# Optimization experiments

Hardware: AMD Instinct MI355X
Metric: run time of the kernel (lower is better)

The kernel has to match this reference:

```python
import jax, jax.numpy as jnp
import numpy as np

B = 16384; HB = 120; BD = 9; NS = 32; NF = 15  # history_bars, bar_descr, n_skills, n_forecast


def _lin_attn(x, wq, wk, wv, wo, bo, g, b):
    # x: [N, S, D_in]; linear attention with phi = elu + 1, residual + LayerNorm
    phi = lambda z: jax.nn.elu(z) + 1.0
    Q = phi(jnp.einsum('nsd,ed->nse', x, wq))
    K = phi(jnp.einsum('nsd,ed->nse', x, wk))
    V = jnp.einsum('nsd,ed->nse', x, wv)
    kv = jnp.einsum('nsd,nse->nde', K, V)              # [N, D, D]
    num = jnp.einsum('nsd,nde->nse', Q, kv)
    den = jnp.maximum(jnp.sum(Q * jnp.sum(K, axis=1, keepdims=True), axis=-1, keepdims=True), 1e-6)
    o = num / den
    y = jnp.einsum('nse,fe->nsf', o, wo) + bo + o      # out_proj + residual
    mu = jnp.mean(y, axis=-1, keepdims=True)
    var = jnp.var(y, axis=-1, keepdims=True)
    return (y - mu) * jax.lax.rsqrt(var + 1e-5) * g + b


def _forward(x, bn_g, bn_b, bn_m, bn_v, wq2, wk2, wv2, wo2, bo2, ln2g, ln2b,
             wq4, wk4, wv4, wo4, bo4, ln4g, ln4b,
             w_ih, w_hh, b_ih, b_hh, cg_w, cg_uw, cg_ub,
             w6, b6, w7, b7, rev_w, rev_b):
    Bn = x.shape[0]
    # BatchNorm1d (eval mode, running stats)
    out = (x - bn_m) * jax.lax.rsqrt(bn_v + 1e-5) * bn_g + bn_b
    # lin_attn_2: tokens = 120 time steps, d = 9 variables
    out = _lin_attn(out.reshape(Bn, HB, BD), wq2, wk2, wv2, wo2, bo2, ln2g, ln2b)
    # transpose_3: [B, 120, 9] -> [B, 9, 120]
    out = jnp.transpose(out, (0, 2, 1))
    # lin_attn_4: 9 parallel sequences of one 120-dim token
    out = _lin_attn(out.reshape(Bn * BD, 1, HB), wq4, wk4, wv4, wo4, bo4, ln4g, ln4b)
    # CGLSTM over 120 steps, vectorized across (batch * 9 variables)
    xs = jnp.transpose(out.reshape(Bn * BD, HB, 1), (1, 0, 2))  # [120, B*9, 1]
    h0 = jnp.zeros((Bn * BD, NS), x.dtype)

    def step(carry, x_t):
        h, c = carry
        gates = x_t @ w_ih.T + b_ih + h @ w_hh.T + b_hh  # [N, 4*NS]
        i, f, g, o = jnp.split(gates, 4, axis=-1)         # torch LSTMCell gate order
        c_new = jax.nn.sigmoid(f) * c + jax.nn.sigmoid(i) * jnp.tanh(g)
        gc = jax.nn.sigmoid(x_t @ cg_w.T + h @ cg_uw.T + cg_ub)  # contextual gate uses old h
        h_new = gc * jnp.tanh(c_new)                      # LSTM's own h output is discarded
        return (h_new, c_new), None

    (h, _), _ = jax.lax.scan(step, (h0, h0), xs)
    cglstm_out = h.reshape(Bn, BD * NS)                   # [B, 288]
    # conv_6 (pointwise per variable) + softplus, conv_7 + tanh
    t = jax.nn.softplus(h @ w6.T + b6)                    # [B*9, 60]
    t = jnp.tanh(t @ w7.T + b7).reshape(Bn, NF * BD)      # [B, 135]
    # transpose_8: view [B,15,9] -> [B,9,15]
    y = jnp.transpose(t.reshape(Bn, NF, BD), (0, 2, 1)).reshape(Bn, -1)
    # RevIN (normalize over full 135-dim vector, unbiased std as in torch.std)
    mu = jnp.mean(y, axis=-1, keepdims=True)
    sd = jnp.maximum(jnp.std(y, axis=-1, keepdims=True, ddof=1), 1e-5)
    enc = (y - mu) / sd * rev_w + rev_b
    return cglstm_out, enc


def setup_inputs() -> dict:
    key = jax.random.key(0)
    ks = jax.random.split(key, 20)
    r = lambda i, s, sc=0.1: jax.random.normal(ks[i], s, jnp.float32) * sc
    return dict(
        x=jax.random.normal(ks[0], (B, HB * BD), jnp.float32),
        bn_g=jnp.ones((HB * BD,), jnp.float32), bn_b=jnp.zeros((HB * BD,), jnp.float32),
        bn_m=r(1, (HB * BD,)),
        bn_v=jax.random.uniform(ks[2], (HB * BD,), jnp.float32, 0.5, 1.5),
        wq2=r(3, (BD, BD), 0.3), wk2=r(4, (BD, BD), 0.3), wv2=r(5, (BD, BD), 0.3),
        wo2=r(6, (BD, BD), 0.3), bo2=jnp.zeros((BD,), jnp.float32),
        ln2g=jnp.ones((BD,), jnp.float32), ln2b=jnp.zeros((BD,), jnp.float32),
        wq4=r(7, (HB, HB), 0.05), wk4=r(8, (HB, HB), 0.05), wv4=r(9, (HB, HB), 0.05),
        wo4=r(10, (HB, HB), 0.05), bo4=jnp.zeros((HB,), jnp.float32),
        ln4g=jnp.ones((HB,), jnp.float32), ln4b=jnp.zeros((HB,), jnp.float32),
        w_ih=r(11, (4 * NS, 1), 0.2), w_hh=r(12, (4 * NS, NS), 0.1),
        b_ih=jnp.zeros((4 * NS,), jnp.float32), b_hh=jnp.zeros((4 * NS,), jnp.float32),
        cg_w=r(13, (NS, 1), 0.2), cg_uw=r(14, (NS, NS), 0.1), cg_ub=jnp.zeros((NS,), jnp.float32),
        w6=r(15, (4 * NF, NS), 0.15), b6=jnp.zeros((4 * NF,), jnp.float32),
        w7=r(16, (NF, 4 * NF), 0.15), b7=jnp.zeros((NF,), jnp.float32),
        rev_w=jnp.ones((BD * NF,), jnp.float32), rev_b=jnp.zeros((BD * NF,), jnp.float32),
    )


def reference(x, bn_g, bn_b, bn_m, bn_v, wq2, wk2, wv2, wo2, bo2, ln2g, ln2b,
              wq4, wk4, wv4, wo4, bo4, ln4g, ln4b,
              w_ih, w_hh, b_ih, b_hh, cg_w, cg_uw, cg_ub,
              w6, b6, w7, b7, rev_w, rev_b):
    return _forward(x, bn_g, bn_b, bn_m, bn_v, wq2, wk2, wv2, wo2, bo2, ln2g, ln2b,
                    wq4, wk4, wv4, wo4, bo4, ln4g, ln4b,
                    w_ih, w_hh, b_ih, b_hh, cg_w, cg_uw, cg_ub,
                    w6, b6, w7, b7, rev_w, rev_b)
```

## Files before the change

kernel.cpp:

```cpp
#include <hip/hip_runtime.h>
#include <math.h>

#define NTH 256
#define SB 7

typedef __attribute__((ext_vector_type(8))) short bf16x8;
typedef __attribute__((ext_vector_type(4))) float f32x4;
typedef __attribute__((ext_vector_type(2))) unsigned short us2;
typedef __attribute__((ext_vector_type(4))) unsigned short us4;

__device__ __forceinline__ float fast_sigmoid(float x) {
    return __builtin_amdgcn_rcpf(1.0f + __expf(-x));
}
__device__ __forceinline__ float fast_tanh(float x) {
    return fmaf(-2.0f, __builtin_amdgcn_rcpf(__expf(2.0f * x) + 1.0f), 1.0f);
}
__device__ __forceinline__ short f2bf(float x) {
    unsigned u = __float_as_uint(x);
    return (short)((u + 0x7FFFu + ((u >> 16) & 1u)) >> 16);
}
__device__ __forceinline__ unsigned pk_bf16(float lo, float hi) {
    unsigned r;
    asm("v_cvt_pk_bf16_f32 %0, %1, %2" : "=v"(r) : "v"(lo), "v"(hi));
    return r;
}
__device__ __forceinline__ float bf2f(unsigned short u) {
    return __uint_as_float(((unsigned)u) << 16);
}

extern "C" __global__ void __launch_bounds__(NTH, 3)
se_kernel(const float* __restrict__ x,
          const float* __restrict__ bn_g, const float* __restrict__ bn_b,
          const float* __restrict__ bn_m, const float* __restrict__ bn_v,
          const float* __restrict__ wq2, const float* __restrict__ wk2,
          const float* __restrict__ wv2, const float* __restrict__ wo2,
          const float* __restrict__ bo2, const float* __restrict__ ln2g,
          const float* __restrict__ ln2b,
          const float* __restrict__ wq4, const float* __restrict__ wk4,
          const float* __restrict__ wv4, const float* __restrict__ wo4,
          const float* __restrict__ bo4, const float* __restrict__ ln4g,
          const float* __restrict__ ln4b,
          const float* __restrict__ w_ih, const float* __restrict__ w_hh,
          const float* __restrict__ b_ih, const float* __restrict__ b_hh,
          const float* __restrict__ cg_w, const float* __restrict__ cg_uw,
          const float* __restrict__ cg_ub,
          const float* __restrict__ w6, const float* __restrict__ b6,
          const float* __restrict__ w7, const float* __restrict__ b7,
          const float* __restrict__ rev_w, const float* __restrict__ rev_b,
          float* __restrict__ out, int Bn)
{
    __shared__ __align__(16) float sm[9862];
    const int tid  = threadIdx.x;
    const int lane = tid & 63;
    const int wv   = tid >> 6;
    const int b0   = blockIdx.x * SB;
    const int nsamp = min(SB, Bn - b0);

    unsigned short* sUb = (unsigned short*)sm;
    float* SCR = sm + 3780;
    float* sKV = sm + 9412; float* sKS = sm + 9493;
    float* sMU = sm + 9412; float* sRS = sm + 9430;
    float* sST = sm + 9448;
    float* sWQ2 = sm + 9502; float* sWK2 = sm + 9583;
    float* sWV2 = sm + 9664; float* sWO2 = sm + 9745;
    float* sBO2 = sm + 9826; float* sLN2G = sm + 9835; float* sLN2B = sm + 9844;
    float* sBO4 = sm + 9502; float* sLN4G = sm + 9622; float* sLN4B = sm + 9742;
    float* sH0 = SCR;
    float* sH1 = SCR + 2816;
    float* sT1 = sm;
    float* sTF = SCR + 2816;

    for (int i = tid; i < 81; i += NTH) {
        sWQ2[i] = wq2[i]; sWK2[i] = wk2[i]; sWV2[i] = wv2[i]; sWO2[i] = wo2[i];
    }
    if (tid < 9) { sBO2[tid] = bo2[tid]; sLN2G[tid] = ln2g[tid]; sLN2B[tid] = ln2b[tid]; }
    __syncthreads();

    float* S0 = SCR; float* S1 = SCR + 1080; float* S2 = SCR + 2160; float* S3 = SCR + 3240;
    for (int ss = 0; ss < SB; ++ss) {
        if (ss < nsamp) {
            const int b = b0 + ss;
            for (int i = tid; i < 1080; i += NTH) {
                float xv = x[(size_t)b * 1080 + i];
                S0[i] = (xv - bn_m[i]) * rsqrtf(bn_v[i] + 1e-5f) * bn_g[i] + bn_b[i];
            }
            __syncthreads();
            for (int idx = tid; idx < 1080; idx += NTH) {
                int s = idx / 9, e = idx - s * 9;
                float aq = 0.f, ak = 0.f, av = 0.f;
                #pragma unroll
                for (int d = 0; d < 9; ++d) {
                    float xv = S0[s * 9 + d];
                    aq = fmaf(xv, sWQ2[e * 9 + d], aq);
                    ak = fmaf(xv, sWK2[e * 9 + d], ak);
                    av = fmaf(xv, sWV2[e * 9 + d], av);
                }
                S1[idx] = aq >= 0.f ? aq + 1.f : __expf(aq);
                S2[idx] = ak >= 0.f ? ak + 1.f : __expf(ak);
                S3[idx] = av;
            }
            __syncthreads();
            if (tid < 81) {
                int d = tid / 9, e = tid - d * 9;
                float acc = 0.f;
                for (int s = 0; s < 120; ++s) acc = fmaf(S2[s * 9 + d], S3[s * 9 + e], acc);
                sKV[tid] = acc;
            } else if (tid < 90) {
                int d = tid - 81;
                float acc = 0.f;
                for (int s = 0; s < 120; ++s) acc += S2[s * 9 + d];
                sKS[d] = acc;
            }
            __syncthreads();
            for (int idx = tid; idx < 1080; idx += NTH) {
                int s = idx / 9, e = idx - s * 9;
                float num = 0.f, den = 0.f;
                #pragma unroll
                for (int d = 0; d < 9; ++d) {
                    float qv = S1[s * 9 + d];
                    num = fmaf(qv, sKV[d * 9 + e], num);
                    den = fmaf(qv, sKS[d], den);
                }
                S0[idx] = num / fmaxf(den, 1e-6f);
            }
            __syncthreads();
            for (int idx = tid; idx < 1080; idx += NTH) {
                int s = idx / 9, f = idx - s * 9;
                float acc = sBO2[f] + S0[s * 9 + f];
                #pragma unroll
                for (int e = 0; e < 9; ++e) acc = fmaf(S0[s * 9 + e], sWO2[f * 9 + e], acc);
                S1[idx] = acc;
            }
            __syncthreads();
            if (tid < 120) {
                int s = tid;
                float sum = 0.f, sq = 0.f;
                #pragma unroll
                for (int f = 0; f < 9; ++f) { float v = S1[s * 9 + f]; sum += v; sq = fmaf(v, v, sq); }
                float mu = sum * (1.f / 9.f);
                float rs = rsqrtf(sq * (1.f / 9.f) - mu * mu + 1e-5f);
                #pragma unroll
                for (int f = 0; f < 9; ++f) {
                    float uo = (S1[s * 9 + f] - mu) * rs * sLN2G[f] + sLN2B[f];
                    sUb[(ss * 9 + f) * 120 + s] = (unsigned short)f2bf(uo);
                }
            }
        }
        __syncthreads();
    }

    for (int i = tid; i < 120; i += NTH) { sBO4[i] = bo4[i]; sLN4G[i] = ln4g[i]; sLN4B[i] = ln4b[i]; }
    for (int p = 0; p < 4; ++p) {
        float* V0 = SCR;
        float* Y0 = SCR + 2160;
        const int sp = tid / 120, erow = tid - sp * 120;
        const int smp = p * 2 + sp;
        const bool act = (tid < 240) && (smp < SB);
        if (act) {
            const unsigned short* uBb = sUb + smp * 1080;
            float acc[9];
            #pragma unroll
            for (int v = 0; v < 9; ++v) acc[v] = 0.f;
            const float* w0p = &wv4[erow * 120];
            for (int dq = 0; dq < 30; ++dq) {
                float4 wA = *(const float4*)&w0p[dq * 4];
                #pragma unroll
                for (int v = 0; v < 9; ++v) {
                    us4 ub = *(const us4*)&uBb[v * 120 + dq * 4];
                    float u0 = bf2f(ub[0]), u1 = bf2f(ub[1]);
                    float u2 = bf2f(ub[2]), u3 = bf2f(ub[3]);
                    acc[v] = fmaf(wA.x, u0, acc[v]); acc[v] = fmaf(wA.y, u1, acc[v]);
                    acc[v] = fmaf(wA.z, u2, acc[v]); acc[v] = fmaf(wA.w, u3, acc[v]);
                }
            }
            float* dst = V0 + sp * 1080;
            #pragma unroll
            for (int v = 0; v < 9; ++v) dst[v * 120 + erow] = acc[v];
        }
        __syncthreads();
        if (act) {
            const float* vB = V0 + sp * 1080;
            float acc[9];
            #pragma unroll
            for (int v = 0; v < 9; ++v) acc[v] = 0.f;
            const float* w0p = &wo4[erow * 120];
            for (int dq = 0; dq < 30; ++dq) {
                float4 wA = *(const float4*)&w0p[dq * 4];
                #pragma unroll
                for (int v = 0; v < 9; ++v) {
                    float4 u = *(const float4*)&vB[v * 120 + dq * 4];
                    acc[v] = fmaf(wA.x, u.x, acc[v]); acc[v] = fmaf(wA.y, u.y, acc[v]);
                    acc[v] = fmaf(wA.z, u.z, acc[v]); acc[v] = fmaf(wA.w, u.w, acc[v]);
                }
            }
            float* Y = Y0 + sp * 1080;
            #pragma unroll
            for (int v = 0; v < 9; ++v)
                Y[v * 120 + erow] = acc[v] + sBO4[erow] + vB[v * 120 + erow];
        }
        __syncthreads();
        if (tid < 18 && (p * 2 + tid / 9) < SB) {
            int sp2 = tid / 9, v = tid - sp2 * 9;
            const float* Y = Y0 + sp2 * 1080 + v * 120;
            float sum = 0.f, sq = 0.f;
            for (int e = 0; e < 120; ++e) { float t = Y[e]; sum += t; sq = fmaf(t, t, sq); }
            float mu = sum * (1.f / 120.f);
            sMU[tid] = mu;
            sRS[tid] = rsqrtf(sq * (1.f / 120.f) - mu * mu + 1e-5f);
        }
        __syncthreads();
        for (int idx = tid; idx < 540; idx += NTH) {
            int sp2 = idx / 270, off = idx - sp2 * 270;
            int smp2 = p * 2 + sp2;
            int v = off / 30, qq = off - v * 30;
            if (smp2 < SB) {
                const float* Y = Y0 + sp2 * 1080;
                float4 y = *(const float4*)&Y[v * 120 + qq * 4];
                float4 g = *(const float4*)&sLN4G[qq * 4];
                float4 bb = *(const float4*)&sLN4B[qq * 4];
                float mu = sMU[sp2 * 9 + v], rs = sRS[sp2 * 9 + v];
                float ox = (y.x - mu) * rs * g.x + bb.x;
                float oy = (y.y - mu) * rs * g.y + bb.y;
                float oz = (y.z - mu) * rs * g.z + bb.z;
                float ow = (y.w - mu) * rs * g.w + bb.w;
                unsigned w0 = pk_bf16(ox, oy), w1 = pk_bf16(oz, ow);
                uint2 pk; pk.x = w0; pk.y = w1;
                *(uint2*)&sUb[(smp2 * 9 + v) * 120 + qq * 4] = pk;
            }
        }
        __syncthreads();
    }

    for (int i = tid; i < 2816; i += NTH) sH0[i] = 0.f;
    __syncthreads();

    const int c = lane & 15, q = lane >> 4;
    bf16x8 bfr[8]; float wxv[8], bsv[8];
    int grow[4]; int pcol;
    {
        bf16x8 pa, pb, pa2, pb2;
        #pragma unroll
        for (int j = 0; j < 8; ++j) { pa[j] = 0; pb[j] = 0; pa2[j] = 0; pb2[j] = 0; }
        if (q == 0) {
            pa[0]  = f2bf((float)c); pb[0]  = f2bf(1.0f);
            pa2[0] = f2bf(1.0f);     pb2[0] = f2bf((float)c);
        }
        f32x4 zc; zc[0] = zc[1] = zc[2] = zc[3] = 0.f;
        f32x4 prr = __builtin_amdgcn_mfma_f32_16x16x32_bf16(pa,  pb,  zc, 0, 0, 0);
        f32x4 pcc = __builtin_amdgcn_mfma_f32_16x16x32_bf16(pa2, pb2, zc, 0, 0, 0);
        #pragma unroll
        for (int r = 0; r < 4; ++r) grow[r] = wv * 16 + (int)(prr[r] + 0.5f);
        pcol = (int)(pcc[0] + 0.5f);

        #pragma unroll
        for (int T = 0; T < 8; ++T) {
            int gate = T >> 1, kk = ((T & 1) << 4) + pcol;
            const float* wr; float wx, bs;
            if (gate < 3) {
                int n = gate * 32 + kk;
                wr = &w_hh[n * 32]; wx = w_ih[n]; bs = b_ih[n] + b_hh[n];
            } else {
                wr = &cg_uw[kk * 32]; wx = cg_w[kk]; bs = cg_ub[kk];
            }
            bf16x8 tv;
            #pragma unroll
            for (int j = 0; j < 8; ++j) tv[j] = f2bf(wr[q * 8 + j]);
            bfr[T] = tv; wxv[T] = wx; bsv[T] = bs;
        }
    }
    float cst[8];
    #pragma unroll
    for (int i = 0; i < 8; ++i) cst[i] = 0.f;
    const int live9 = nsamp * 9;
    const float* ar0 = &sH0[(wv * 16 + c) * 44 + q * 8];
    const float* ar1 = &sH1[(wv * 16 + c) * 44 + q * 8];

#define LSTM_STEP(RP, WPL, XARR)                                               \
    {                                                                          \
        float4 hA = *(const float4*)(RP);                                      \
        float4 hB = *(const float4*)((RP) + 4);                                \
        union { unsigned u[4]; bf16x8 v; } afu;                                \
        afu.u[0] = pk_bf16(hA.x, hA.y);                                        \
        afu.u[1] = pk_bf16(hA.z, hA.w);                                        \
        afu.u[2] = pk_bf16(hB.x, hB.y);                                        \
        afu.u[3] = pk_bf16(hB.z, hB.w);                                        \
        f32x4 acc[8];                                                          \
        _Pragma("unroll")                                                      \
        for (int T = 0; T < 8; ++T) {                                          \
            f32x4 ci;                                                          \
            _Pragma("unroll")                                                  \
            for (int r = 0; r < 4; ++r) ci[r] = fmaf(wxv[T], XARR[r], bsv[T]); \
            acc[T] = __builtin_amdgcn_mfma_f32_16x16x32_bf16(afu.v, bfr[T], ci, 0, 0, 0); \
        }                                                                      \
        _Pragma("unroll")                                                      \
        for (int kh = 0; kh < 2; ++kh) {                                       \
            _Pragma("unroll")                                                  \
            for (int r = 0; r < 4; ++r) {                                      \
                float si  = fast_sigmoid(acc[kh][r]);                          \
                float sf  = fast_sigmoid(acc[2 + kh][r]);                      \
                float tg  = fast_tanh(acc[4 + kh][r]);                         \
                float sgc = fast_sigmoid(acc[6 + kh][r]);                      \
                float cn = fmaf(sf, cst[kh * 4 + r], si * tg);                 \
                cst[kh * 4 + r] = cn;                                          \
                (WPL)[grow[r] * 44 + (kh << 4) + pcol] = sgc * fast_tanh(cn);  \
            }                                                                  \
        }                                                                      \
    }

    for (int t = 0; t < 120; t += 2) {
        float xa[4], xb[4];
        #pragma unroll
        for (int r = 0; r < 4; ++r) {
            if (grow[r] < live9) {
                us2 xv = *(const us2*)&sUb[grow[r] * 120 + t];
                xa[r] = bf2f(xv[0]); xb[r] = bf2f(xv[1]);
            } else { xa[r] = 0.f; xb[r] = 0.f; }
        }
        LSTM_STEP(ar0, sH1, xa)
        LSTM_STEP(ar1, sH0, xb)
    }
    __syncthreads();

    for (int idx = tid; idx < SB * 288; idx += NTH) {
        int ssd = idx / 288, r = idx - ssd * 288;
        if (ssd < nsamp) {
            int v = r >> 5, k = r & 31;
            out[(size_t)(b0 + ssd) * 288 + r] = sH0[(ssd * 9 + v) * 44 + k];
        }
    }

    for (int idx = tid; idx < SB * 540; idx += NTH) {
        int ssd = idx / 540, rem = idx - ssd * 540;
        int v = rem / 60, j = rem - v * 60;
        if (ssd < nsamp) {
            float acc = b6[j];
            const float4* wr4 = (const float4*)&w6[j * 32];
            const float4* hv = (const float4*)&sH0[(ssd * 9 + v) * 44];
            #pragma unroll
            for (int qq = 0; qq < 8; ++qq) {
                float4 w = wr4[qq], h = hv[qq];
                acc = fmaf(w.x, h.x, acc); acc = fmaf(w.y, h.y, acc);
                acc = fmaf(w.z, h.z, acc); acc = fmaf(w.w, h.w, acc);
            }
            sT1[idx] = acc > 15.f ? acc : log1pf(__expf(acc));
        }
    }
    __syncthreads();
    for (int idx = tid; idx < SB * 135; idx += NTH) {
        int ssd = idx / 135, rem = idx - ssd * 135;
        int v = rem / 15, f = rem - v * 15;
        if (ssd < nsamp) {
            float acc = b7[f];
            const float4* wr = (const float4*)&w7[f * 60];
            const float4* tv = (const float4*)&sT1[ssd * 540 + v * 60];
            #pragma unroll
            for (int qq = 0; qq < 15; ++qq) {
                float4 w = wr[qq], h = tv[qq];
                acc = fmaf(w.x, h.x, acc); acc = fmaf(w.y, h.y, acc);
                acc = fmaf(w.z, h.z, acc); acc = fmaf(w.w, h.w, acc);
            }
            sTF[idx] = fast_tanh(acc);
        }
    }
    __syncthreads();
    if (tid < SB && tid < nsamp) {
        const float* tf = &sTF[tid * 135];
        float sum = 0.f;
        for (int i = 0; i < 135; ++i) sum += tf[i];
        float mu = sum * (1.f / 135.f);
        float sq = 0.f;
        for (int i = 0; i < 135; ++i) { float d = tf[i] - mu; sq = fmaf(d, d, sq); }
        float sd = sqrtf(sq * (1.f / 134.f));
        sST[tid * 2]     = mu;
        sST[tid * 2 + 1] = 1.f / fmaxf(sd, 1e-5f);
    }
    __syncthreads();
    const size_t encbase = (size_t)Bn * 288;
    for (int idx = tid; idx < SB * 135; idx += NTH) {
        int ssd = idx / 135, j = idx - ssd * 135;
        if (ssd < nsamp) {
            int qq = j / 15, pp = j - qq * 15;
            float val = (sTF[ssd * 135 + pp * 9 + qq] - sST[ssd * 2]) * sST[ssd * 2 + 1] * rev_w[j] + rev_b[j];
            out[encbase + (size_t)(b0 + ssd) * 135 + j] = val;
        }
    }
}

extern "C" void kernel_launch(void* const* d_in, const int* in_sizes, int n_in,
                              void* d_out, int out_size, void* d_ws, size_t ws_size,
                              hipStream_t stream) {
    const float* x    = (const float*)d_in[0];
    const float* bn_g = (const float*)d_in[1];
    const float* bn_b = (const float*)d_in[2];
    const float* bn_m = (const float*)d_in[3];
    const float* bn_v = (const float*)d_in[4];
    const float* wq2  = (const float*)d_in[5];
    const float* wk2  = (const float*)d_in[6];
    const float* wv2  = (const float*)d_in[7];
    const float* wo2  = (const float*)d_in[8];
    const float* bo2  = (const float*)d_in[9];
    const float* ln2g = (const float*)d_in[10];
    const float* ln2b = (const float*)d_in[11];
    const float* wq4  = (const float*)d_in[12];
    const float* wk4  = (const float*)d_in[13];
    const float* wv4  = (const float*)d_in[14];
    const float* wo4  = (const float*)d_in[15];
    const float* bo4  = (const float*)d_in[16];
    const float* ln4g = (const float*)d_in[17];
    const float* ln4b = (const float*)d_in[18];
    const float* w_ih = (const float*)d_in[19];
    const float* w_hh = (const float*)d_in[20];
    const float* b_ih = (const float*)d_in[21];
    const float* b_hh = (const float*)d_in[22];
    const float* cg_w = (const float*)d_in[23];
    const float* cg_uw= (const float*)d_in[24];
    const float* cg_ub= (const float*)d_in[25];
    const float* w6   = (const float*)d_in[26];
    const float* b6   = (const float*)d_in[27];
    const float* w7   = (const float*)d_in[28];
    const float* b7   = (const float*)d_in[29];
    const float* rev_w= (const float*)d_in[30];
    const float* rev_b= (const float*)d_in[31];

    int Bn = in_sizes[0] / 1080;
    int grid = (Bn + SB - 1) / SB;
    hipLaunchKernelGGL(se_kernel, dim3(grid), dim3(NTH), 0, stream,
                       x, bn_g, bn_b, bn_m, bn_v, wq2, wk2, wv2, wo2, bo2, ln2g, ln2b,
                       wq4, wk4, wv4, wo4, bo4, ln4g, ln4b,
                       w_ih, w_hh, b_ih, b_hh, cg_w, cg_uw, cg_ub,
                       w6, b6, w7, b7, rev_w, rev_b,
                       (float*)d_out, Bn);
}
```

Baseline: 1.321 ms.

## Store attention intermediates and LSTM hidden state in bf16 to shrink LDS

Converts the Q/K/V scratch buffers, the lin_attn_4 V buffer and the LSTM hidden-state ping-pong buffers from fp32 to bf16 in shared memory. The LDS footprint drops from about 39 KB to about 30 KB per block, which may let more blocks reside per CU. The LSTM step now loads a bf16x8 MFMA operand directly instead of converting fp32 to bf16 every step, which removes pack instructions from the serial recurrence. The cost is added bf16 rounding in the KV/Q and V intermediates and in the final hidden-state output, which lowers accuracy.

```diff
diff --git a/kernel.cpp b/kernel.cpp
--- a/kernel.cpp
+++ b/kernel.cpp
@@ -49,7 +49,7 @@
           const float* __restrict__ rev_w, const float* __restrict__ rev_b,
           float* __restrict__ out, int Bn)
 {
-    __shared__ __align__(16) float sm[9862];
+    __shared__ __align__(16) float sm[7470];
     const int tid  = threadIdx.x;
     const int lane = tid & 63;
     const int wv   = tid >> 6;
@@ -58,17 +58,24 @@
 
     unsigned short* sUb = (unsigned short*)sm;
     float* SCR = sm + 3780;
-    float* sKV = sm + 9412; float* sKS = sm + 9493;
-    float* sMU = sm + 9412; float* sRS = sm + 9430;
-    float* sST = sm + 9448;
-    float* sWQ2 = sm + 9502; float* sWK2 = sm + 9583;
-    float* sWV2 = sm + 9664; float* sWO2 = sm + 9745;
-    float* sBO2 = sm + 9826; float* sLN2G = sm + 9835; float* sLN2B = sm + 9844;
-    float* sBO4 = sm + 9502; float* sLN4G = sm + 9622; float* sLN4B = sm + 9742;
-    float* sH0 = SCR;
-    float* sH1 = SCR + 2816;
+    float* S0 = SCR;
+    unsigned short* S1b = (unsigned short*)(SCR + 1080);
+    unsigned short* S2b = (unsigned short*)(SCR + 1620);
+    unsigned short* S3b = (unsigned short*)(SCR + 2160);
+    float* SY = SCR + 1080;
+    unsigned short* Vb = (unsigned short*)SCR;
+    float* Y0 = SCR + 1080;
+    unsigned short* sH0b = (unsigned short*)SCR;
+    unsigned short* sH1b = (unsigned short*)(SCR + 1536);
+    float* sKV = sm + 7020; float* sKS = sm + 7101;
+    float* sMU = sm + 7020; float* sRS = sm + 7038;
+    float* sST = sm + 7056;
+    float* sWQ2 = sm + 7110; float* sWK2 = sm + 7191;
+    float* sWV2 = sm + 7272; float* sWO2 = sm + 7353;
+    float* sBO2 = sm + 7434; float* sLN2G = sm + 7443; float* sLN2B = sm + 7452;
+    float* sBO4 = sm + 7110; float* sLN4G = sm + 7230; float* sLN4B = sm + 7350;
     float* sT1 = sm;
-    float* sTF = SCR + 2816;
+    float* sTF = SCR;
 
     for (int i = tid; i < 81; i += NTH) {
         sWQ2[i] = wq2[i]; sWK2[i] = wk2[i]; sWV2[i] = wv2[i]; sWO2[i] = wo2[i];
@@ -76,7 +83,6 @@
     if (tid < 9) { sBO2[tid] = bo2[tid]; sLN2G[tid] = ln2g[tid]; sLN2B[tid] = ln2b[tid]; }
     __syncthreads();
 
-    float* S0 = SCR; float* S1 = SCR + 1080; float* S2 = SCR + 2160; float* S3 = SCR + 3240;
     for (int ss = 0; ss < SB; ++ss) {
         if (ss < nsamp) {
             const int b = b0 + ss;
@@ -95,20 +101,21 @@
                     ak = fmaf(xv, sWK2[e * 9 + d], ak);
                     av = fmaf(xv, sWV2[e * 9 + d], av);
                 }
-                S1[idx] = aq >= 0.f ? aq + 1.f : __expf(aq);
-                S2[idx] = ak >= 0.f ? ak + 1.f : __expf(ak);
-                S3[idx] = av;
+                S1b[idx] = (unsigned short)f2bf(aq >= 0.f ? aq + 1.f : __expf(aq));
+                S2b[idx] = (unsigned short)f2bf(ak >= 0.f ? ak + 1.f : __expf(ak));
+                S3b[idx] = (unsigned short)f2bf(av);
             }
             __syncthreads();
             if (tid < 81) {
                 int d = tid / 9, e = tid - d * 9;
                 float acc = 0.f;
-                for (int s = 0; s < 120; ++s) acc = fmaf(S2[s * 9 + d], S3[s * 9 + e], acc);
+                for (int s = 0; s < 120; ++s)
+                    acc = fmaf(bf2f(S2b[s * 9 + d]), bf2f(S3b[s * 9 + e]), acc);
                 sKV[tid] = acc;
             } else if (tid < 90) {
                 int d = tid - 81;
                 float acc = 0.f;
-                for (int s = 0; s < 120; ++s) acc += S2[s * 9 + d];
+                for (int s = 0; s < 120; ++s) acc += bf2f(S2b[s * 9 + d]);
                 sKS[d] = acc;
             }
             __syncthreads();
@@ -117,7 +124,7 @@
                 float num = 0.f, den = 0.f;
                 #pragma unroll
                 for (int d = 0; d < 9; ++d) {
-                    float qv = S1[s * 9 + d];
+                    float qv = bf2f(S1b[s * 9 + d]);
                     num = fmaf(qv, sKV[d * 9 + e], num);
                     den = fmaf(qv, sKS[d], den);
                 }
@@ -129,19 +136,19 @@
                 float acc = sBO2[f] + S0[s * 9 + f];
                 #pragma unroll
                 for (int e = 0; e < 9; ++e) acc = fmaf(S0[s * 9 + e], sWO2[f * 9 + e], acc);
-                S1[idx] = acc;
+                SY[idx] = acc;
             }
             __syncthreads();
             if (tid < 120) {
                 int s = tid;
                 float sum = 0.f, sq = 0.f;
                 #pragma unroll
-                for (int f = 0; f < 9; ++f) { float v = S1[s * 9 + f]; sum += v; sq = fmaf(v, v, sq); }
+                for (int f = 0; f < 9; ++f) { float v = SY[s * 9 + f]; sum += v; sq = fmaf(v, v, sq); }
                 float mu = sum * (1.f / 9.f);
                 float rs = rsqrtf(sq * (1.f / 9.f) - mu * mu + 1e-5f);
                 #pragma unroll
                 for (int f = 0; f < 9; ++f) {
-                    float uo = (S1[s * 9 + f] - mu) * rs * sLN2G[f] + sLN2B[f];
+                    float uo = (SY[s * 9 + f] - mu) * rs * sLN2G[f] + sLN2B[f];
                     sUb[(ss * 9 + f) * 120 + s] = (unsigned short)f2bf(uo);
                 }
             }
@@ -151,8 +158,6 @@
 
     for (int i = tid; i < 120; i += NTH) { sBO4[i] = bo4[i]; sLN4G[i] = ln4g[i]; sLN4B[i] = ln4b[i]; }
     for (int p = 0; p < 4; ++p) {
-        float* V0 = SCR;
-        float* Y0 = SCR + 2160;
         const int sp = tid / 120, erow = tid - sp * 120;
         const int smp = p * 2 + sp;
         const bool act = (tid < 240) && (smp < SB);
@@ -167,19 +172,19 @@
                 #pragma unroll
                 for (int v = 0; v < 9; ++v) {
                     us4 ub = *(const us4*)&uBb[v * 120 + dq * 4];
-                    float u0 = bf2f(ub[0]), u1 = bf2f(ub[1]);
-                    float u2 = bf2f(ub[2]), u3 = bf2f(ub[3]);
-                    acc[v] = fmaf(wA.x, u0, acc[v]); acc[v] = fmaf(wA.y, u1, acc[v]);
-                    acc[v] = fmaf(wA.z, u2, acc[v]); acc[v] = fmaf(wA.w, u3, acc[v]);
+                    acc[v] = fmaf(wA.x, bf2f(ub[0]), acc[v]);
+                    acc[v] = fmaf(wA.y, bf2f(ub[1]), acc[v]);
+                    acc[v] = fmaf(wA.z, bf2f(ub[2]), acc[v]);
+                    acc[v] = fmaf(wA.w, bf2f(ub[3]), acc[v]);
                 }
             }
-            float* dst = V0 + sp * 1080;
-            #pragma unroll
-            for (int v = 0; v < 9; ++v) dst[v * 120 + erow] = acc[v];
+            unsigned short* dst = Vb + sp * 1080;
+            #pragma unroll
+            for (int v = 0; v < 9; ++v) dst[v * 120 + erow] = (unsigned short)f2bf(acc[v]);
         }
         __syncthreads();
         if (act) {
-            const float* vB = V0 + sp * 1080;
+            const unsigned short* vBb = Vb + sp * 1080;
             float acc[9];
             #pragma unroll
             for (int v = 0; v < 9; ++v) acc[v] = 0.f;
@@ -188,15 +193,17 @@
                 float4 wA = *(const float4*)&w0p[dq * 4];
                 #pragma unroll
                 for (int v = 0; v < 9; ++v) {
-                    float4 u = *(const float4*)&vB[v * 120 + dq * 4];
-                    acc[v] = fmaf(wA.x, u.x, acc[v]); acc[v] = fmaf(wA.y, u.y, acc[v]);
-                    acc[v] = fmaf(wA.z, u.z, acc[v]); acc[v] = fmaf(wA.w, u.w, acc[v]);
+                    us4 ub = *(const us4*)&vBb[v * 120 + dq * 4];
+                    acc[v] = fmaf(wA.x, bf2f(ub[0]), acc[v]);
+                    acc[v] = fmaf(wA.y, bf2f(ub[1]), acc[v]);
+                    acc[v] = fmaf(wA.z, bf2f(ub[2]), acc[v]);
+                    acc[v] = fmaf(wA.w, bf2f(ub[3]), acc[v]);
                 }
             }
             float* Y = Y0 + sp * 1080;
             #pragma unroll
             for (int v = 0; v < 9; ++v)
-                Y[v * 120 + erow] = acc[v] + sBO4[erow] + vB[v * 120 + erow];
+                Y[v * 120 + erow] = acc[v] + sBO4[erow] + bf2f(vBb[v * 120 + erow]);
         }
         __syncthreads();
         if (tid < 18 && (p * 2 + tid / 9) < SB) {
@@ -223,15 +230,14 @@
                 float oy = (y.y - mu) * rs * g.y + bb.y;
                 float oz = (y.z - mu) * rs * g.z + bb.z;
                 float ow = (y.w - mu) * rs * g.w + bb.w;
-                unsigned w0 = pk_bf16(ox, oy), w1 = pk_bf16(oz, ow);
-                uint2 pk; pk.x = w0; pk.y = w1;
+                uint2 pk; pk.x = pk_bf16(ox, oy); pk.y = pk_bf16(oz, ow);
                 *(uint2*)&sUb[(smp2 * 9 + v) * 120 + qq * 4] = pk;
             }
         }
         __syncthreads();
     }
 
-    for (int i = tid; i < 2816; i += NTH) sH0[i] = 0.f;
+    for (int i = tid; i < 1536; i += NTH) ((float*)sH0b)[i] = 0.f;
     __syncthreads();
 
     const int c = lane & 15, q = lane >> 4;
@@ -272,26 +278,21 @@
     #pragma unroll
     for (int i = 0; i < 8; ++i) cst[i] = 0.f;
     const int live9 = nsamp * 9;
-    const float* ar0 = &sH0[(wv * 16 + c) * 44 + q * 8];
-    const float* ar1 = &sH1[(wv * 16 + c) * 44 + q * 8];
+    const unsigned short* ar0 = &sH0b[(wv * 16 + c) * 48 + q * 8];
+    const unsigned short* ar1 = &sH1b[(wv * 16 + c) * 48 + q * 8];
 
 #define LSTM_STEP(RP, WPL, XARR)                                               \
     {                                                                          \
-        float4 hA = *(const float4*)(RP);                                      \
-        float4 hB = *(const float4*)((RP) + 4);                                \
-        union { unsigned u[4]; bf16x8 v; } afu;                                \
-        afu.u[0] = pk_bf16(hA.x, hA.y);                                        \
-        afu.u[1] = pk_bf16(hA.z, hA.w);                                        \
-        afu.u[2] = pk_bf16(hB.x, hB.y);                                        \
-        afu.u[3] = pk_bf16(hB.z, hB.w);                                        \
+        bf16x8 af = *(const bf16x8*)(RP);                                      \
         f32x4 acc[8];                                                          \
         _Pragma("unroll")                                                      \
         for (int T = 0; T < 8; ++T) {                                          \
             f32x4 ci;                                                          \
             _Pragma("unroll")                                                  \
             for (int r = 0; r < 4; ++r) ci[r] = fmaf(wxv[T], XARR[r], bsv[T]); \
-            acc[T] = __builtin_amdgcn_mfma_f32_16x16x32_bf16(afu.v, bfr[T], ci, 0, 0, 0); \
+            acc[T] = __builtin_amdgcn_mfma_f32_16x16x32_bf16(af, bfr[T], ci, 0, 0, 0); \
         }                                                                      \
+        float ho[8];                                                           \
         _Pragma("unroll")                                                      \
         for (int kh = 0; kh < 2; ++kh) {                                       \
             _Pragma("unroll")                                                  \
@@ -302,8 +303,14 @@
                 float sgc = fast_sigmoid(acc[6 + kh][r]);                      \
                 float cn = fmaf(sf, cst[kh * 4 + r], si * tg);                 \
                 cst[kh * 4 + r] = cn;                                          \
-                (WPL)[grow[r] * 44 + (kh << 4) + pcol] = sgc * fast_tanh(cn);  \
+                ho[kh * 4 + r] = sgc * fast_tanh(cn);                          \
             }                                                                  \
+        }                                                                      \
+        _Pragma("unroll")                                                      \
+        for (int r = 0; r < 4; ++r) {                                          \
+            unsigned u = pk_bf16(ho[r], ho[4 + r]);                            \
+            (WPL)[grow[r] * 48 + pcol]      = (unsigned short)(u & 0xffffu);   \
+            (WPL)[grow[r] * 48 + 16 + pcol] = (unsigned short)(u >> 16);       \
         }                                                                      \
     }
 
@@ -316,8 +323,8 @@
                 xa[r] = bf2f(xv[0]); xb[r] = bf2f(xv[1]);
             } else { xa[r] = 0.f; xb[r] = 0.f; }
         }
-        LSTM_STEP(ar0, sH1, xa)
-        LSTM_STEP(ar1, sH0, xb)
+        LSTM_STEP(ar0, sH1b, xa)
+        LSTM_STEP(ar1, sH0b, xb)
     }
     __syncthreads();
 
@@ -325,7 +332,7 @@
         int ssd = idx / 288, r = idx - ssd * 288;
         if (ssd < nsamp) {
             int v = r >> 5, k = r & 31;
-            out[(size_t)(b0 + ssd) * 288 + r] = sH0[(ssd * 9 + v) * 44 + k];
+            out[(size_t)(b0 + ssd) * 288 + r] = bf2f(sH0b[(ssd * 9 + v) * 48 + k]);
         }
     }
 
@@ -335,12 +342,13 @@
         if (ssd < nsamp) {
             float acc = b6[j];
             const float4* wr4 = (const float4*)&w6[j * 32];
-            const float4* hv = (const float4*)&sH0[(ssd * 9 + v) * 44];
+            const unsigned short* hrow = &sH0b[(ssd * 9 + v) * 48];
             #pragma unroll
             for (int qq = 0; qq < 8; ++qq) {
-                float4 w = wr4[qq], h = hv[qq];
-                acc = fmaf(w.x, h.x, acc); acc = fmaf(w.y, h.y, acc);
-                acc = fmaf(w.z, h.z, acc); acc = fmaf(w.w, h.w, acc);
+                float4 w = wr4[qq];
+                us4 hb = *(const us4*)&hrow[qq * 4];
+                acc = fmaf(w.x, bf2f(hb[0]), acc); acc = fmaf(w.y, bf2f(hb[1]), acc);
+                acc = fmaf(w.z, bf2f(hb[2]), acc); acc = fmaf(w.w, bf2f(hb[3]), acc);
             }
             sT1[idx] = acc > 15.f ? acc : log1pf(__expf(acc));
         }
```

Measured after the change: 1.401 ms. +6.0%, slower.
